# Performance work log

Measured on AMD Instinct MI355X. Metric: run time of the kernel, lower is better.

Reference implementation:

```python
import jax, jax.numpy as jnp
import numpy as np

B, L, E, H, V = 32, 2048, 512, 512, 32000  # batch, encoder_len, tar_emb, hid_dim, vocab


def setup_inputs() -> dict:
    key = jax.random.key(0)
    ks = jax.random.split(key, 16)
    w = lambda k, shape: (jax.random.normal(k, shape, jnp.float32) * 0.05)
    emb = w(ks[0], (V, E)).at[0].set(0.0)  # padding_idx=0
    return {
        "x": jax.random.randint(ks[1], (B,), 0, V),
        "h": jax.random.normal(ks[2], (2, B, H), jnp.float32),
        "encoder_out": jax.random.normal(ks[3], (B, L, 2 * H), jnp.float32),
        "emb": emb,
        "attn_W": w(ks[4], (1, 4 * H + E)),
        "attn_b": jnp.zeros((1,), jnp.float32),
        "W_ih_f": w(ks[5], (3 * H, 2 * H)),
        "W_hh_f": w(ks[6], (3 * H, H)),
        "b_ih_f": jnp.zeros((3 * H,), jnp.float32),
        "b_hh_f": jnp.zeros((3 * H,), jnp.float32),
        "W_ih_b": w(ks[7], (3 * H, 2 * H)),
        "W_hh_b": w(ks[8], (3 * H, H)),
        "b_ih_b": jnp.zeros((3 * H,), jnp.float32),
        "b_hh_b": jnp.zeros((3 * H,), jnp.float32),
        "out_W": w(ks[9], (V, 2 * H)),
        "out_b": jnp.zeros((V,), jnp.float32),
    }


def _gru_cell(x, h, W_ih, W_hh, b_ih, b_hh):
    gi = x @ W_ih.T + b_ih          # [B, 3H]
    gh = h @ W_hh.T + b_hh          # [B, 3H]
    i_r, i_z, i_n = jnp.split(gi, 3, axis=-1)
    h_r, h_z, h_n = jnp.split(gh, 3, axis=-1)
    r = jax.nn.sigmoid(i_r + h_r)
    z = jax.nn.sigmoid(i_z + h_z)
    n = jnp.tanh(i_n + r * h_n)
    return (1.0 - z) * n + z * h


def reference(x, h, encoder_out, emb, attn_W, attn_b,
              W_ih_f, W_hh_f, b_ih_f, b_hh_f,
              W_ih_b, W_hh_b, b_ih_b, b_hh_b,
              out_W, out_b):
    x_emb = emb[x]                                     # [B, E]
    Bsz = encoder_out.shape[0]
    prev_h = jnp.transpose(h, (1, 0, 2)).reshape(Bsz, -1)  # [B, 2H]
    # Vectorized equivalent of the per-timestep concat+Linear loop:
    # split attn weight over the concatenated [x_emb, prev_h, enc_t] segments.
    Wx = attn_W[:, :E]                 # [1, E]
    Wp = attn_W[:, E:E + 2 * H]        # [1, 2H]
    We = attn_W[:, E + 2 * H:]         # [1, 2H]
    base = x_emb @ Wx.T + prev_h @ Wp.T + attn_b       # [B, 1]
    scores = base + jnp.einsum('bld,od->bl', encoder_out, We)  # [B, L]
    # Faithful: original applies softmax over the singleton dim of each [B,1]
    # score -> betas are all ones (zero gradient into scores).
    betas = jax.nn.softmax(scores[..., None], axis=-1)[..., 0]  # [B, L] (== 1)
    attn_weights = jax.nn.softmax(betas, axis=1)                # [B, L]
    c = jnp.einsum('bl,bld->bd', attn_weights, encoder_out)     # [B, 2H]
    # n_layers = 1: relu then one bidirectional GRU step (seq_len == 1)
    c = jax.nn.relu(c)
    h_f = _gru_cell(c, h[0], W_ih_f, W_hh_f, b_ih_f, b_hh_f)
    h_b = _gru_cell(c, h[1], W_ih_b, W_hh_b, b_ih_b, b_hh_b)
    c_out = jnp.concatenate([h_f, h_b], axis=-1)       # [B, 2H]
    h_new = jnp.stack([h_f, h_b], axis=0)              # [2, B, H]
    # Faithful: c[-1] in torch indexes the batch dim of [B,1,2H] -> [1,2H]
    logits = c_out[-1:] @ out_W.T + out_b              # [1, V]
    logp = jax.nn.log_softmax(logits, axis=-1)
    return (logp, h_new, attn_weights)
```

## Files before the change

### kernel.cpp

```cpp
#include <hip/hip_runtime.h>
#include <math.h>


#define NCH 32

__global__ __launch_bounds__(256) void k1_enc(const float* __restrict__ enc,
                                              float* __restrict__ partial,
                                              float* __restrict__ out,
                                              float* __restrict__ Sbins) {
  const int bid = blockIdx.x, tid = threadIdx.x;
  if (bid < 1024) {
    const int ch = bid & 31, b = bid >> 5;
    const float4* src = (const float4*)enc + ((size_t)b * 2048 + (size_t)ch * 64) * 256 + tid;
    float4 acc = make_float4(0.f, 0.f, 0.f, 0.f);
#pragma unroll 8
    for (int l = 0; l < 64; ++l) {
      float4 v = src[(size_t)l * 256];
      acc.x += v.x; acc.y += v.y; acc.z += v.z; acc.w += v.w;
    }
    ((float4*)partial)[((size_t)b * NCH + ch) * 256 + tid] = acc;
  } else if (bid < 1088) {
    const int i4 = (bid - 1024) * 256 + tid;
    const float w = 1.0f / 2048.0f;
    ((float4*)out)[16192 + i4] = make_float4(w, w, w, w);
  } else {
    if (tid < 64) Sbins[tid] = 0.f;
  }
}

__global__ __launch_bounds__(256) void k2_c(const float* __restrict__ partial,
                                            float* __restrict__ c) {
  __shared__ float4 red[4][64];
  const int tid = threadIdx.x;
  const int col = tid & 63;
  const int q   = tid >> 6;
  const int g   = blockIdx.x * 64 + col;
  const int b = g >> 8, d4 = g & 255;
  const float4* p4 = (const float4*)partial + (size_t)b * NCH * 256 + d4;
  float4 s = make_float4(0.f, 0.f, 0.f, 0.f);
#pragma unroll
  for (int j = 0; j < 8; ++j) {
    float4 v = p4[(size_t)(q * 8 + j) * 256];
    s.x += v.x; s.y += v.y; s.z += v.z; s.w += v.w;
  }
  red[q][col] = s;
  __syncthreads();
  if (tid < 64) {
    float4 a = red[0][tid], b2 = red[1][tid], c2 = red[2][tid], d2 = red[3][tid];
    const float sc = 1.0f / 2048.0f;
    float x = a.x + b2.x + c2.x + d2.x;
    float y = a.y + b2.y + c2.y + d2.y;
    float z = a.z + b2.z + c2.z + d2.z;
    float w = a.w + b2.w + c2.w + d2.w;
    float4 r;
    r.x = x > 0.f ? x * sc : 0.f;
    r.y = y > 0.f ? y * sc : 0.f;
    r.z = z > 0.f ? z * sc : 0.f;
    r.w = w > 0.f ? w * sc : 0.f;
    ((float4*)c)[blockIdx.x * 64 + tid] = r;
  }
}

__device__ __forceinline__ void gru_waves(
    int wid, int lane, int b_lo, int b_hi,
    const float* __restrict__ c, const float* __restrict__ h,
    const float* __restrict__ Wih_f, const float* __restrict__ Whh_f,
    const float* __restrict__ bih_f, const float* __restrict__ bhh_f,
    const float* __restrict__ Wih_b, const float* __restrict__ Whh_b,
    const float* __restrict__ bih_b, const float* __restrict__ bhh_b,
    float* __restrict__ out) {
  const int dir = wid >> 9;
  const int k   = wid & 511;
  const float* Wih = dir ? Wih_b : Wih_f;
  const float* Whh = dir ? Whh_b : Whh_f;
  const float* bih = dir ? bih_b : bih_f;
  const float* bhh = dir ? bhh_b : bhh_f;
  const float4* Wih4 = (const float4*)Wih;
  const float4* Whh4 = (const float4*)Whh;

  float4 wr[4], wz[4], wn[4];
#pragma unroll
  for (int i = 0; i < 4; ++i) {
    wr[i] = Wih4[(size_t)k * 256 + i * 64 + lane];
    wz[i] = Wih4[(size_t)(k + 512) * 256 + i * 64 + lane];
    wn[i] = Wih4[(size_t)(k + 1024) * 256 + i * 64 + lane];
  }
  float4 ur[2], uz[2], un[2];
#pragma unroll
  for (int i = 0; i < 2; ++i) {
    ur[i] = Whh4[(size_t)k * 128 + i * 64 + lane];
    uz[i] = Whh4[(size_t)(k + 512) * 128 + i * 64 + lane];
    un[i] = Whh4[(size_t)(k + 1024) * 128 + i * 64 + lane];
  }
  const float bkr = bih[k], bkz = bih[k + 512], bkn = bih[k + 1024];
  const float ckr = bhh[k], ckz = bhh[k + 512], ckn = bhh[k + 1024];

  const float4* c4 = (const float4*)c;
  const float4* h4 = (const float4*)h + (size_t)dir * 32 * 128;

  for (int b = b_lo; b < b_hi; ++b) {
    float pr = 0.f, pz = 0.f, pn = 0.f;
#pragma unroll
    for (int i = 0; i < 4; ++i) {
      float4 v = c4[b * 256 + i * 64 + lane];
      pr += v.x * wr[i].x + v.y * wr[i].y + v.z * wr[i].z + v.w * wr[i].w;
      pz += v.x * wz[i].x + v.y * wz[i].y + v.z * wz[i].z + v.w * wz[i].w;
      pn += v.x * wn[i].x + v.y * wn[i].y + v.z * wn[i].z + v.w * wn[i].w;
    }
    float qr = 0.f, qz = 0.f, qn = 0.f;
#pragma unroll
    for (int i = 0; i < 2; ++i) {
      float4 v = h4[b * 128 + i * 64 + lane];
      qr += v.x * ur[i].x + v.y * ur[i].y + v.z * ur[i].z + v.w * ur[i].w;
      qz += v.x * uz[i].x + v.y * uz[i].y + v.z * uz[i].z + v.w * uz[i].w;
      qn += v.x * un[i].x + v.y * un[i].y + v.z * un[i].z + v.w * un[i].w;
    }
#pragma unroll
    for (int off = 32; off; off >>= 1) {
      pr += __shfl_xor(pr, off, 64);
      pz += __shfl_xor(pz, off, 64);
      pn += __shfl_xor(pn, off, 64);
      qr += __shfl_xor(qr, off, 64);
      qz += __shfl_xor(qz, off, 64);
      qn += __shfl_xor(qn, off, 64);
    }
    if (lane == 0) {
      float r = 1.f / (1.f + expf(-(pr + bkr + qr + ckr)));
      float z = 1.f / (1.f + expf(-(pz + bkz + qz + ckz)));
      float n = tanhf(pn + bkn + r * (qn + ckn));
      float hp = h[(size_t)dir * 32 * 512 + (size_t)b * 512 + k];
      out[32000 + dir * 16384 + b * 512 + k] = (1.f - z) * n + z * hp;
    }
  }
}

__global__ __launch_bounds__(256) void k3_gru31(
    const float* __restrict__ c, const float* __restrict__ h,
    const float* __restrict__ Wih_f, const float* __restrict__ Whh_f,
    const float* __restrict__ bih_f, const float* __restrict__ bhh_f,
    const float* __restrict__ Wih_b, const float* __restrict__ Whh_b,
    const float* __restrict__ bih_b, const float* __restrict__ bhh_b,
    float* __restrict__ out) {
  const int lane = threadIdx.x & 63;
  const int wid  = (blockIdx.x * 256 + threadIdx.x) >> 6;
  gru_waves(wid, lane, 31, 32, c, h, Wih_f, Whh_f, bih_f, bhh_f,
            Wih_b, Whh_b, bih_b, bhh_b, out);
}

__global__ __launch_bounds__(256) void k4_logits_gru(
    const float* __restrict__ outW, const float* __restrict__ outb,
    const float* __restrict__ dout_ro, float* __restrict__ logits,
    float* __restrict__ Sbins,
    const float* __restrict__ c, const float* __restrict__ h,
    const float* __restrict__ Wih_f, const float* __restrict__ Whh_f,
    const float* __restrict__ bih_f, const float* __restrict__ bhh_f,
    const float* __restrict__ Wih_b, const float* __restrict__ Whh_b,
    const float* __restrict__ bih_b, const float* __restrict__ bhh_b,
    float* __restrict__ out) {
  __shared__ float se[4];
  const int tid = threadIdx.x, lane = tid & 63;
  if (blockIdx.x < 8000) {
    const int v = (blockIdx.x * 256 + tid) >> 6;
    const float4* hf = (const float4*)(dout_ro + 32000 + 31 * 512);
    const float4* hb = (const float4*)(dout_ro + 32000 + 16384 + 31 * 512);
    const float4* W4 = (const float4*)outW + (size_t)v * 256;
    float p = 0.f;
#pragma unroll
    for (int i = 0; i < 4; ++i) {
      const int pos = i * 64 + lane;
      float4 cv = (pos < 128) ? hf[pos] : hb[pos - 128];
      float4 wv = W4[pos];
      p += cv.x * wv.x + cv.y * wv.y + cv.z * wv.z + cv.w * wv.w;
    }
#pragma unroll
    for (int off = 32; off; off >>= 1) p += __shfl_xor(p, off, 64);
    if (lane == 0) {
      float l = p + outb[v];
      logits[v] = l;
      se[tid >> 6] = expf(l);
    }
    __syncthreads();
    if (tid == 0) atomicAdd(&Sbins[blockIdx.x & 63], se[0] + se[1] + se[2] + se[3]);
  } else {
    const int wid = ((blockIdx.x - 8000) * 256 + tid) >> 6;
    gru_waves(wid, lane, 0, 31, c, h, Wih_f, Whh_f, bih_f, bhh_f,
              Wih_b, Whh_b, bih_b, bhh_b, out);
  }
}

__global__ __launch_bounds__(256) void k5_tail(const float* __restrict__ logits,
                                               const float* __restrict__ Sbins,
                                               float* __restrict__ out) {
  __shared__ float s_ls;
  const int tid = threadIdx.x;
  if (tid < 64) {
    float s = Sbins[tid];
#pragma unroll
    for (int off = 32; off; off >>= 1) s += __shfl_xor(s, off, 64);
    if (tid == 0) s_ls = logf(s);
  }
  __syncthreads();
  const float ls = s_ls;
  if (tid < 250) {
    const int i4 = blockIdx.x * 250 + tid;
    float4 v = ((const float4*)logits)[i4];
    ((float4*)out)[i4] = make_float4(v.x - ls, v.y - ls, v.z - ls, v.w - ls);
  }
}

extern "C" void kernel_launch(void* const* d_in, const int* in_sizes, int n_in,
                              void* d_out, int out_size, void* d_ws, size_t ws_size,
                              hipStream_t stream) {
  const float* h     = (const float*)d_in[1];
  const float* enc   = (const float*)d_in[2];
  const float* Wih_f = (const float*)d_in[6];
  const float* Whh_f = (const float*)d_in[7];
  const float* bih_f = (const float*)d_in[8];
  const float* bhh_f = (const float*)d_in[9];
  const float* Wih_b = (const float*)d_in[10];
  const float* Whh_b = (const float*)d_in[11];
  const float* bih_b = (const float*)d_in[12];
  const float* bhh_b = (const float*)d_in[13];
  const float* outW  = (const float*)d_in[14];
  const float* outb  = (const float*)d_in[15];
  float* out = (float*)d_out;
  float* ws  = (float*)d_ws;

  float* partial = ws;
  float* cbuf    = partial + 32 * NCH * 1024;
  float* logits  = cbuf + 32768;
  float* Sbins   = logits + 32000;

  k1_enc<<<1089, 256, 0, stream>>>(enc, partial, out, Sbins);
  k2_c<<<128, 256, 0, stream>>>(partial, cbuf);
  k3_gru31<<<256, 256, 0, stream>>>(cbuf, h, Wih_f, Whh_f, bih_f, bhh_f,
                                    Wih_b, Whh_b, bih_b, bhh_b, out);
  k4_logits_gru<<<8256, 256, 0, stream>>>(outW, outb, out, logits, Sbins,
                                          cbuf, h, Wih_f, Whh_f, bih_f, bhh_f,
                                          Wih_b, Whh_b, bih_b, bhh_b, out);
  k5_tail<<<32, 256, 0, stream>>>(logits, Sbins, out);
}
```

Measured before the change: 561.1 us.

## Split GRU from logits kernel and spread softmax atomics over more bins

Before this change, the GRU for batch row 31 ran on its own and the other 31 rows were overlapped inside the logits kernel. Now a single GRU kernel computes all 32 rows first, and the logits kernel runs afterwards as a standalone launch. The logits kernel drops the shared-memory block reduction and syncthreads and does one atomicAdd per wave into 256 bins instead of 64. The GRU also folds the hidden-side r and z partial sums into the input-side ones, so each step needs fewer shuffle reductions. The risk is that the GRU work is now serialized ahead of the memory-bound logits pass instead of overlapping with it, and the logits kernel issues four times as many atomics.

```diff
diff --git a/kernel.cpp b/kernel.cpp
--- a/kernel.cpp
+++ b/kernel.cpp
@@ -3,6 +3,7 @@
 
 
 #define NCH 32
+#define NBIN 256
 
 __global__ __launch_bounds__(256) void k1_enc(const float* __restrict__ enc,
                                               float* __restrict__ partial,
@@ -24,7 +25,7 @@
     const float w = 1.0f / 2048.0f;
     ((float4*)out)[16192 + i4] = make_float4(w, w, w, w);
   } else {
-    if (tid < 64) Sbins[tid] = 0.f;
+    Sbins[tid] = 0.f;
   }
 }
 
@@ -61,80 +62,7 @@
   }
 }
 
-__device__ __forceinline__ void gru_waves(
-    int wid, int lane, int b_lo, int b_hi,
-    const float* __restrict__ c, const float* __restrict__ h,
-    const float* __restrict__ Wih_f, const float* __restrict__ Whh_f,
-    const float* __restrict__ bih_f, const float* __restrict__ bhh_f,
-    const float* __restrict__ Wih_b, const float* __restrict__ Whh_b,
-    const float* __restrict__ bih_b, const float* __restrict__ bhh_b,
-    float* __restrict__ out) {
-  const int dir = wid >> 9;
-  const int k   = wid & 511;
-  const float* Wih = dir ? Wih_b : Wih_f;
-  const float* Whh = dir ? Whh_b : Whh_f;
-  const float* bih = dir ? bih_b : bih_f;
-  const float* bhh = dir ? bhh_b : bhh_f;
-  const float4* Wih4 = (const float4*)Wih;
-  const float4* Whh4 = (const float4*)Whh;
-
-  float4 wr[4], wz[4], wn[4];
-#pragma unroll
-  for (int i = 0; i < 4; ++i) {
-    wr[i] = Wih4[(size_t)k * 256 + i * 64 + lane];
-    wz[i] = Wih4[(size_t)(k + 512) * 256 + i * 64 + lane];
-    wn[i] = Wih4[(size_t)(k + 1024) * 256 + i * 64 + lane];
-  }
-  float4 ur[2], uz[2], un[2];
-#pragma unroll
-  for (int i = 0; i < 2; ++i) {
-    ur[i] = Whh4[(size_t)k * 128 + i * 64 + lane];
-    uz[i] = Whh4[(size_t)(k + 512) * 128 + i * 64 + lane];
-    un[i] = Whh4[(size_t)(k + 1024) * 128 + i * 64 + lane];
-  }
-  const float bkr = bih[k], bkz = bih[k + 512], bkn = bih[k + 1024];
-  const float ckr = bhh[k], ckz = bhh[k + 512], ckn = bhh[k + 1024];
-
-  const float4* c4 = (const float4*)c;
-  const float4* h4 = (const float4*)h + (size_t)dir * 32 * 128;
-
-  for (int b = b_lo; b < b_hi; ++b) {
-    float pr = 0.f, pz = 0.f, pn = 0.f;
-#pragma unroll
-    for (int i = 0; i < 4; ++i) {
-      float4 v = c4[b * 256 + i * 64 + lane];
-      pr += v.x * wr[i].x + v.y * wr[i].y + v.z * wr[i].z + v.w * wr[i].w;
-      pz += v.x * wz[i].x + v.y * wz[i].y + v.z * wz[i].z + v.w * wz[i].w;
-      pn += v.x * wn[i].x + v.y * wn[i].y + v.z * wn[i].z + v.w * wn[i].w;
-    }
-    float qr = 0.f, qz = 0.f, qn = 0.f;
-#pragma unroll
-    for (int i = 0; i < 2; ++i) {
-      float4 v = h4[b * 128 + i * 64 + lane];
-      qr += v.x * ur[i].x + v.y * ur[i].y + v.z * ur[i].z + v.w * ur[i].w;
-      qz += v.x * uz[i].x + v.y * uz[i].y + v.z * uz[i].z + v.w * uz[i].w;
-      qn += v.x * un[i].x + v.y * un[i].y + v.z * un[i].z + v.w * un[i].w;
-    }
-#pragma unroll
-    for (int off = 32; off; off >>= 1) {
-      pr += __shfl_xor(pr, off, 64);
-      pz += __shfl_xor(pz, off, 64);
-      pn += __shfl_xor(pn, off, 64);
-      qr += __shfl_xor(qr, off, 64);
-      qz += __shfl_xor(qz, off, 64);
-      qn += __shfl_xor(qn, off, 64);
-    }
-    if (lane == 0) {
-      float r = 1.f / (1.f + expf(-(pr + bkr + qr + ckr)));
-      float z = 1.f / (1.f + expf(-(pz + bkz + qz + ckz)));
-      float n = tanhf(pn + bkn + r * (qn + ckn));
-      float hp = h[(size_t)dir * 32 * 512 + (size_t)b * 512 + k];
-      out[32000 + dir * 16384 + b * 512 + k] = (1.f - z) * n + z * hp;
-    }
-  }
-}
-
-__global__ __launch_bounds__(256) void k3_gru31(
+__global__ __launch_bounds__(256) void k_gru(
     const float* __restrict__ c, const float* __restrict__ h,
     const float* __restrict__ Wih_f, const float* __restrict__ Whh_f,
     const float* __restrict__ bih_f, const float* __restrict__ bhh_f,
@@ -143,62 +71,113 @@
     float* __restrict__ out) {
   const int lane = threadIdx.x & 63;
   const int wid  = (blockIdx.x * 256 + threadIdx.x) >> 6;
-  gru_waves(wid, lane, 31, 32, c, h, Wih_f, Whh_f, bih_f, bhh_f,
-            Wih_b, Whh_b, bih_b, bhh_b, out);
-}
-
-__global__ __launch_bounds__(256) void k4_logits_gru(
-    const float* __restrict__ outW, const float* __restrict__ outb,
-    const float* __restrict__ dout_ro, float* __restrict__ logits,
-    float* __restrict__ Sbins,
-    const float* __restrict__ c, const float* __restrict__ h,
-    const float* __restrict__ Wih_f, const float* __restrict__ Whh_f,
-    const float* __restrict__ bih_f, const float* __restrict__ bhh_f,
-    const float* __restrict__ Wih_b, const float* __restrict__ Whh_b,
-    const float* __restrict__ bih_b, const float* __restrict__ bhh_b,
-    float* __restrict__ out) {
-  __shared__ float se[4];
-  const int tid = threadIdx.x, lane = tid & 63;
-  if (blockIdx.x < 8000) {
-    const int v = (blockIdx.x * 256 + tid) >> 6;
-    const float4* hf = (const float4*)(dout_ro + 32000 + 31 * 512);
-    const float4* hb = (const float4*)(dout_ro + 32000 + 16384 + 31 * 512);
-    const float4* W4 = (const float4*)outW + (size_t)v * 256;
-    float p = 0.f;
+  const int dir  = wid >> 9;
+  const int k    = wid & 511;
+  const float* Wih = dir ? Wih_b : Wih_f;
+  const float* Whh = dir ? Whh_b : Whh_f;
+  const float* bih = dir ? bih_b : bih_f;
+  const float* bhh = dir ? bhh_b : bhh_f;
+  const float4* Wih4 = (const float4*)Wih;
+  const float4* Whh4 = (const float4*)Whh;
+
+  float4 wr[4], wz[4], wn[4];
+#pragma unroll
+  for (int i = 0; i < 4; ++i) {
+    wr[i] = Wih4[(size_t)k * 256 + i * 64 + lane];
+    wz[i] = Wih4[(size_t)(k + 512) * 256 + i * 64 + lane];
+    wn[i] = Wih4[(size_t)(k + 1024) * 256 + i * 64 + lane];
+  }
+  float4 ur[2], uz[2], un[2];
+#pragma unroll
+  for (int i = 0; i < 2; ++i) {
+    ur[i] = Whh4[(size_t)k * 128 + i * 64 + lane];
+    uz[i] = Whh4[(size_t)(k + 512) * 128 + i * 64 + lane];
+    un[i] = Whh4[(size_t)(k + 1024) * 128 + i * 64 + lane];
+  }
+  const float bkr = bih[k], bkz = bih[k + 512], bkn = bih[k + 1024];
+  const float ckr = bhh[k], ckz = bhh[k + 512], ckn = bhh[k + 1024];
+
+  const float4* c4 = (const float4*)c;
+  const float4* h4 = (const float4*)h + (size_t)dir * 32 * 128;
+
+  for (int b = 0; b < 32; ++b) {
+    float pr = 0.f, pz = 0.f, pn = 0.f;
 #pragma unroll
     for (int i = 0; i < 4; ++i) {
-      const int pos = i * 64 + lane;
-      float4 cv = (pos < 128) ? hf[pos] : hb[pos - 128];
-      float4 wv = W4[pos];
-      p += cv.x * wv.x + cv.y * wv.y + cv.z * wv.z + cv.w * wv.w;
-    }
-#pragma unroll
-    for (int off = 32; off; off >>= 1) p += __shfl_xor(p, off, 64);
+      float4 v = c4[b * 256 + i * 64 + lane];
+      pr += v.x * wr[i].x + v.y * wr[i].y + v.z * wr[i].z + v.w * wr[i].w;
+      pz += v.x * wz[i].x + v.y * wz[i].y + v.z * wz[i].z + v.w * wz[i].w;
+      pn += v.x * wn[i].x + v.y * wn[i].y + v.z * wn[i].z + v.w * wn[i].w;
+    }
+    float qn = 0.f;
+    {
+      float qr = 0.f, qz = 0.f;
+#pragma unroll
+      for (int i = 0; i < 2; ++i) {
+        float4 v = h4[b * 128 + i * 64 + lane];
+        qr += v.x * ur[i].x + v.y * ur[i].y + v.z * ur[i].z + v.w * ur[i].w;
+        qz += v.x * uz[i].x + v.y * uz[i].y + v.z * uz[i].z + v.w * uz[i].w;
+        qn += v.x * un[i].x + v.y * un[i].y + v.z * un[i].z + v.w * un[i].w;
+      }
+      pr += qr;
+      pz += qz;
+    }
+#pragma unroll
+    for (int off = 32; off; off >>= 1) {
+      pr += __shfl_xor(pr, off, 64);
+      pz += __shfl_xor(pz, off, 64);
+      pn += __shfl_xor(pn, off, 64);
+      qn += __shfl_xor(qn, off, 64);
+    }
     if (lane == 0) {
-      float l = p + outb[v];
-      logits[v] = l;
-      se[tid >> 6] = expf(l);
-    }
-    __syncthreads();
-    if (tid == 0) atomicAdd(&Sbins[blockIdx.x & 63], se[0] + se[1] + se[2] + se[3]);
-  } else {
-    const int wid = ((blockIdx.x - 8000) * 256 + tid) >> 6;
-    gru_waves(wid, lane, 0, 31, c, h, Wih_f, Whh_f, bih_f, bhh_f,
-              Wih_b, Whh_b, bih_b, bhh_b, out);
+      float r = 1.f / (1.f + expf(-(pr + bkr + ckr)));
+      float z = 1.f / (1.f + expf(-(pz + bkz + ckz)));
+      float n = tanhf(pn + bkn + r * (qn + ckn));
+      float hp = h[(size_t)dir * 32 * 512 + (size_t)b * 512 + k];
+      out[32000 + dir * 16384 + b * 512 + k] = (1.f - z) * n + z * hp;
+    }
+  }
+}
+
+__global__ __launch_bounds__(256) void k4_logits(const float* __restrict__ outW,
+                                                 const float* __restrict__ outb,
+                                                 const float* __restrict__ dout,
+                                                 float* __restrict__ logits,
+                                                 float* __restrict__ Sbins) {
+  const int lane = threadIdx.x & 63;
+  const int v = (blockIdx.x * 256 + threadIdx.x) >> 6;
+  const float4* hf = (const float4*)(dout + 32000 + 31 * 512);
+  const float4* hb = (const float4*)(dout + 32000 + 16384 + 31 * 512);
+  const float4* W4 = (const float4*)outW + (size_t)v * 256;
+  float p = 0.f;
+#pragma unroll
+  for (int i = 0; i < 4; ++i) {
+    const int pos = i * 64 + lane;
+    float4 cv = (pos < 128) ? hf[pos] : hb[pos - 128];
+    float4 wv = W4[pos];
+    p += cv.x * wv.x + cv.y * wv.y + cv.z * wv.z + cv.w * wv.w;
+  }
+#pragma unroll
+  for (int off = 32; off; off >>= 1) p += __shfl_xor(p, off, 64);
+  if (lane == 0) {
+    const float l = p + outb[v];
+    logits[v] = l;
+    atomicAdd(&Sbins[v & (NBIN - 1)], expf(l));
   }
 }
 
 __global__ __launch_bounds__(256) void k5_tail(const float* __restrict__ logits,
                                                const float* __restrict__ Sbins,
                                                float* __restrict__ out) {
+  __shared__ float red[4];
   __shared__ float s_ls;
-  const int tid = threadIdx.x;
-  if (tid < 64) {
-    float s = Sbins[tid];
-#pragma unroll
-    for (int off = 32; off; off >>= 1) s += __shfl_xor(s, off, 64);
-    if (tid == 0) s_ls = logf(s);
-  }
+  const int tid = threadIdx.x, lane = tid & 63, w = tid >> 6;
+  float s = Sbins[tid];
+#pragma unroll
+  for (int off = 32; off; off >>= 1) s += __shfl_xor(s, off, 64);
+  if (lane == 0) red[w] = s;
+  __syncthreads();
+  if (tid == 0) s_ls = logf(red[0] + red[1] + red[2] + red[3]);
   __syncthreads();
   const float ls = s_ls;
   if (tid < 250) {
@@ -233,10 +212,8 @@
 
   k1_enc<<<1089, 256, 0, stream>>>(enc, partial, out, Sbins);
   k2_c<<<128, 256, 0, stream>>>(partial, cbuf);
-  k3_gru31<<<256, 256, 0, stream>>>(cbuf, h, Wih_f, Whh_f, bih_f, bhh_f,
-                                    Wih_b, Whh_b, bih_b, bhh_b, out);
-  k4_logits_gru<<<8256, 256, 0, stream>>>(outW, outb, out, logits, Sbins,
-                                          cbuf, h, Wih_f, Whh_f, bih_f, bhh_f,
-                                          Wih_b, Whh_b, bih_b, bhh_b, out);
+  k_gru<<<256, 256, 0, stream>>>(cbuf, h, Wih_f, Whh_f, bih_f, bhh_f,
+                                 Wih_b, Whh_b, bih_b, bhh_b, out);
+  k4_logits<<<8000, 256, 0, stream>>>(outW, outb, out, logits, Sbins);
   k5_tail<<<32, 256, 0, stream>>>(logits, Sbins, out);
 }
```

Measured after the change: 578.2 us. 3.1% more time.
